# Kernel tuning notes

Hardware: AMD Instinct MI355X
Metric: run time of the kernel (lower is better)

Reference implementation:

```python
import jax, jax.numpy as jnp
import numpy as np

B, L = 4, 1024
D_IN, D_MODEL, DEPTH = 8, 512, 4
D_INNER, D_STATE, D_CONV = 2 * D_MODEL, 16, 4
DT_RANK = (D_MODEL + 15) // 16  # 32


def setup_inputs():
    key = jax.random.key(0)
    ks = jax.random.split(key, 12)
    s = 0.02
    inp = {
        "x": jax.random.normal(ks[0], (B, L, D_IN), jnp.float32),
        "in_w": jax.random.normal(ks[1], (D_MODEL, D_IN), jnp.float32) * s,
        "in_b": jnp.zeros((D_MODEL,), jnp.float32),
        "W_xz": jax.random.normal(ks[2], (DEPTH, 2 * D_INNER, D_MODEL), jnp.float32) * s,
        "conv_w": jax.random.normal(ks[3], (DEPTH, D_INNER, D_CONV), jnp.float32) * 0.1,
        "conv_b": jnp.zeros((DEPTH, D_INNER), jnp.float32),
        "W_xp": jax.random.normal(ks[4], (DEPTH, DT_RANK + 2 * D_STATE, D_INNER), jnp.float32) * s,
        "W_dt": jax.random.normal(ks[5], (DEPTH, D_INNER, DT_RANK), jnp.float32) * 0.1,
        "b_dt": jax.random.uniform(ks[6], (DEPTH, D_INNER), jnp.float32, -4.0, -2.0),
        "A_log": jnp.broadcast_to(jnp.log(jnp.arange(1, D_STATE + 1, dtype=jnp.float32)), (DEPTH, D_INNER, D_STATE)) + 0.0,
        "D_param": jnp.ones((DEPTH, D_INNER), jnp.float32),
        "W_out": jax.random.normal(ks[7], (DEPTH, D_MODEL, D_INNER), jnp.float32) * s,
        "ln_g": jnp.ones((D_MODEL,), jnp.float32),
        "ln_b": jnp.zeros((D_MODEL,), jnp.float32),
    }
    return inp


def _silu(x):
    return x * jax.nn.sigmoid(x)


def _mamba_layer(h, Wxz, cw, cb, Wxp, Wdt, bdt, A_log, Dp, Wout):
    # in_proj -> (x, z)
    xz = jnp.einsum('bld,ed->ble', h, Wxz)           # (B,L,2*D_INNER)
    xc, z = jnp.split(xz, 2, axis=-1)
    # causal depthwise conv1d, kernel D_CONV
    xp = jnp.pad(xc, ((0, 0), (D_CONV - 1, 0), (0, 0)))
    xconv = sum(xp[:, k:k + L, :] * cw[:, k] for k in range(D_CONV)) + cb
    u = _silu(xconv)                                 # (B,L,D_INNER)
    # x_proj -> dt, B, C
    xdbl = jnp.einsum('bld,ed->ble', u, Wxp)
    dt_lr = xdbl[..., :DT_RANK]
    Bm = xdbl[..., DT_RANK:DT_RANK + D_STATE]        # (B,L,D_STATE)
    Cm = xdbl[..., DT_RANK + D_STATE:]               # (B,L,D_STATE)
    dt = jax.nn.softplus(jnp.einsum('blr,dr->bld', dt_lr, Wdt) + bdt)  # (B,L,D_INNER)
    A = -jnp.exp(A_log)                              # (D_INNER,D_STATE)

    def step(hst, inp):
        dt_t, B_t, C_t, u_t = inp                    # (B,Di),(B,S),(B,S),(B,Di)
        dA = jnp.exp(dt_t[..., None] * A)            # (B,Di,S)
        dBu = dt_t[..., None] * B_t[:, None, :] * u_t[..., None]
        hst = dA * hst + dBu
        y_t = jnp.einsum('bds,bs->bd', hst, C_t)
        return hst, y_t

    h0 = jnp.zeros((h.shape[0], D_INNER, D_STATE), h.dtype)
    xs = (dt.transpose(1, 0, 2), Bm.transpose(1, 0, 2), Cm.transpose(1, 0, 2), u.transpose(1, 0, 2))
    _, ys = jax.lax.scan(step, h0, xs)
    y = ys.transpose(1, 0, 2) + u * Dp               # (B,L,D_INNER)
    y = y * _silu(z)
    return jnp.einsum('ble,de->bld', y, Wout)


def reference(x, in_w, in_b, W_xz, conv_w, conv_b, W_xp, W_dt, b_dt, A_log, D_param, W_out, ln_g, ln_b):
    h = jnp.einsum('bli,di->bld', x, in_w) + in_b
    for i in range(DEPTH):
        h = _mamba_layer(h, W_xz[i], conv_w[i], conv_b[i], W_xp[i], W_dt[i], b_dt[i], A_log[i], D_param[i], W_out[i])
    mu = h.mean(-1, keepdims=True)
    var = ((h - mu) ** 2).mean(-1, keepdims=True)
    return (h - mu) * jax.lax.rsqrt(var + 1e-5) * ln_g + ln_b
```

## Files before the change

### kernel.cpp

```cpp
#include <hip/hip_runtime.h>
#include <math.h>

#define B_      4
#define L_      1024
#define D_INNC  8
#define DMODEL  512
#define DEPTH_  4
#define DINNER  1024
#define DSTATE  16
#define DCONV   4
#define DTRANK  32
#define MTOT    (B_*L_)
#define CHUNKS  64
#define CLEN    16
#define XPSPLIT 8

typedef float f32x4 __attribute__((ext_vector_type(4)));
typedef short s16x8 __attribute__((ext_vector_type(8)));
typedef unsigned short u16;
typedef unsigned short u16x4v __attribute__((ext_vector_type(4)));

__device__ __forceinline__ u16 f2bf(float v) {
    unsigned b = __float_as_uint(v);
    return (u16)((b + 0x7FFF + ((b >> 16) & 1)) >> 16);
}
__device__ __forceinline__ float bf2f(u16 h) {
    return __uint_as_float((unsigned)h << 16);
}

__global__ __launch_bounds__(256) void in_proj_kernel(
    const float* __restrict__ x, const float* __restrict__ w,
    const float* __restrict__ bias, u16* __restrict__ hb)
{
    int idx = blockIdx.x * 256 + threadIdx.x;
    int m = idx / DMODEL, d = idx % DMODEL;
    const float* xr = x + m * D_INNC;
    const float* wr = w + d * D_INNC;
    float acc = bias[d];
#pragma unroll
    for (int k = 0; k < D_INNC; ++k) acc += xr[k] * wr[k];
    hb[idx] = f2bf(acc);
}

__global__ __launch_bounds__(256) void wconv_kernel(
    const float* __restrict__ W, u16* __restrict__ Wb)
{
    int i = blockIdx.x * 256 + threadIdx.x;
    const float* src = W + (size_t)i * 8;
    float4 f0 = *(const float4*)src;
    float4 f1 = *(const float4*)(src + 4);
    float f[8] = {f0.x,f0.y,f0.z,f0.w,f1.x,f1.y,f1.z,f1.w};
    s16x8 hv;
#pragma unroll
    for (int e = 0; e < 8; ++e) hv[e] = (short)f2bf(f[e]);
    *(s16x8*)(Wb + (size_t)i * 8) = hv;
}

template<int BM, int BN, int MODE>
__global__ __launch_bounds__(256, 2) void gemm_bf16(
    const u16* __restrict__ A, int lda,
    const u16* __restrict__ B, int ldb,
    void* __restrict__ C0, void* __restrict__ C1,
    int ldc, int K)
{
    constexpr int FM  = BM / 32;
    constexpr int FN  = BN / 32;
    constexpr int ACH = BM / 64;
    constexpr int BCH = BN / 64;
    __shared__ __align__(16) u16 As[4*(BM+1)*8];
    __shared__ __align__(16) u16 Bs[4*(BN+1)*8];

    const int t    = threadIdx.x;
    const int lane = t & 63;
    const int w    = t >> 6;
    const int wm   = (w >> 1) * (BM / 2);
    const int wn   = (w & 1) * (BN / 2);
    const int quad = lane >> 4;
    const int l16  = lane & 15;
    const int m0   = blockIdx.y * BM;
    const int n0   = (MODE == 6) ? 0 : blockIdx.x * BN;
    const int kbase= (MODE == 6) ? blockIdx.x * K : 0;

    f32x4 acc[FM][FN];
#pragma unroll
    for (int i = 0; i < FM; ++i)
#pragma unroll
        for (int j = 0; j < FN; ++j) acc[i][j] = (f32x4){0.f,0.f,0.f,0.f};

    s16x8 ra[ACH], rb[BCH];
#pragma unroll
    for (int c = 0; c < ACH; ++c) {
        int id = c*256 + t, row = id >> 2, kb = id & 3;
        ra[c] = *(const s16x8*)(A + (size_t)(m0 + row) * lda + kbase + kb*8);
    }
#pragma unroll
    for (int c = 0; c < BCH; ++c) {
        int id = c*256 + t, row = id >> 2, kb = id & 3;
        rb[c] = *(const s16x8*)(B + (size_t)(n0 + row) * ldb + kbase + kb*8);
    }

    for (int kk = 0; kk < K; kk += 32) {
        __syncthreads();
#pragma unroll
        for (int c = 0; c < ACH; ++c) {
            int id = c*256 + t, row = id >> 2, kb = id & 3;
            *(s16x8*)&As[(kb*(BM+1) + row) * 8] = ra[c];
        }
#pragma unroll
        for (int c = 0; c < BCH; ++c) {
            int id = c*256 + t, row = id >> 2, kb = id & 3;
            *(s16x8*)&Bs[(kb*(BN+1) + row) * 8] = rb[c];
        }
        __syncthreads();
        int kn = kk + 32;
        if (kn < K) {
#pragma unroll
            for (int c = 0; c < ACH; ++c) {
                int id = c*256 + t, row = id >> 2, kb = id & 3;
                ra[c] = *(const s16x8*)(A + (size_t)(m0 + row) * lda + kbase + kn + kb*8);
            }
#pragma unroll
            for (int c = 0; c < BCH; ++c) {
                int id = c*256 + t, row = id >> 2, kb = id & 3;
                rb[c] = *(const s16x8*)(B + (size_t)(n0 + row) * ldb + kbase + kn + kb*8);
            }
        }
        s16x8 afr[FM], bfr[FN];
#pragma unroll
        for (int i = 0; i < FM; ++i)
            afr[i] = *(const s16x8*)&As[(quad*(BM+1) + wm + i*16 + l16) * 8];
#pragma unroll
        for (int j = 0; j < FN; ++j)
            bfr[j] = *(const s16x8*)&Bs[(quad*(BN+1) + wn + j*16 + l16) * 8];
#pragma unroll
        for (int i = 0; i < FM; ++i)
#pragma unroll
            for (int j = 0; j < FN; ++j)
                acc[i][j] = __builtin_amdgcn_mfma_f32_16x16x32_bf16(afr[i], bfr[j], acc[i][j], 0, 0, 0);
    }

    if constexpr (MODE == 2) {
        u16* C = (u16*)C0;
#pragma unroll
        for (int i = 0; i < FM; ++i)
#pragma unroll
            for (int j = 0; j < FN; ++j) {
                int col = n0 + wn + j*16 + l16;
#pragma unroll
                for (int r = 0; r < 4; ++r) {
                    int row = m0 + wm + i*16 + quad*4 + r;
                    C[(size_t)row * ldc + col] = f2bf(acc[i][j][r]);
                }
            }
    } else if constexpr (MODE == 6) {
        float* P = (float*)C0 + (size_t)blockIdx.x * MTOT * 64;
#pragma unroll
        for (int i = 0; i < FM; ++i)
#pragma unroll
            for (int j = 0; j < FN; ++j) {
                int col = wn + j*16 + l16;
#pragma unroll
                for (int r = 0; r < 4; ++r) {
                    int row = m0 + wm + i*16 + quad*4 + r;
                    P[(size_t)row * 64 + col] = acc[i][j][r];
                }
            }
    } else if constexpr (MODE == 4) {
        u16* dtb_ = (u16*)C0;
        const float* bdt = (const float*)C1;
#pragma unroll
        for (int i = 0; i < FM; ++i)
#pragma unroll
            for (int j = 0; j < FN; ++j) {
                int col = n0 + wn + j*16 + l16;
                float bb = bdt[col];
#pragma unroll
                for (int r = 0; r < 4; ++r) {
                    int row = m0 + wm + i*16 + quad*4 + r;
                    float v = acc[i][j][r] + bb;
                    float sp = (v > 20.f) ? v : log1pf(__expf(v));
                    dtb_[(size_t)row * ldc + col] = f2bf(sp);
                }
            }
    } else {
        u16* xcb = (u16*)C0;
        u16* szb = (u16*)C1;
#pragma unroll
        for (int i = 0; i < FM; ++i)
#pragma unroll
            for (int j = 0; j < FN; ++j) {
                int col = n0 + wn + j*16 + l16;
                bool isz = col >= DINNER;
                int cc = col & (DINNER - 1);
                u16* dst = isz ? szb : xcb;
#pragma unroll
                for (int r = 0; r < 4; ++r) {
                    int row = m0 + wm + i*16 + quad*4 + r;
                    float v = acc[i][j][r];
                    if (isz) v = v / (1.f + __expf(-v));
                    dst[(size_t)row * DINNER + cc] = f2bf(v);
                }
            }
    }
}

__global__ __launch_bounds__(256) void xpred_kernel(
    const float* __restrict__ part, u16* __restrict__ dtlr,
    float* __restrict__ xd)
{
    int tid = blockIdx.x * 256 + threadIdx.x;
    int m = tid >> 4, c4 = (tid & 15) * 4;
    float s0 = 0.f, s1 = 0.f, s2 = 0.f, s3 = 0.f;
#pragma unroll
    for (int p = 0; p < XPSPLIT; ++p) {
        float4 v = *(const float4*)&part[((size_t)p * MTOT + m) * 64 + c4];
        s0 += v.x; s1 += v.y; s2 += v.z; s3 += v.w;
    }
    if (c4 < 32) {
        u16x4v o;
        o[0] = f2bf(s0); o[1] = f2bf(s1); o[2] = f2bf(s2); o[3] = f2bf(s3);
        *(u16x4v*)&dtlr[(size_t)m * 32 + c4] = o;
    } else {
        float4 o; o.x = s0; o.y = s1; o.z = s2; o.w = s3;
        *(float4*)&xd[(size_t)m * 64 + c4] = o;
    }
}

__global__ __launch_bounds__(256) void conv_silu_kernel(
    const u16* __restrict__ xcb, const float* __restrict__ cw,
    const float* __restrict__ cb, u16* __restrict__ ub)
{
    int idx = (blockIdx.x * 256 + threadIdx.x) * 2;
    int m = idx >> 10;
    int d = idx & (DINNER - 1);
    int l = m & (L_ - 1);

    const float4 w0 = *(const float4*)&cw[d * 4];
    const float4 w1 = *(const float4*)&cw[(d + 1) * 4];
    float a0 = cb[d], a1 = cb[d + 1];
#pragma unroll
    for (int k = 0; k < 4; ++k) {
        int lag = 3 - k;
        if (l >= lag) {
            unsigned v = *(const unsigned*)&xcb[(size_t)(m - lag) * DINNER + d];
            float x0 = bf2f((u16)(v & 0xffff));
            float x1 = bf2f((u16)(v >> 16));
            float wk0 = (&w0.x)[k], wk1 = (&w1.x)[k];
            a0 += x0 * wk0; a1 += x1 * wk1;
        }
    }
    a0 = a0 / (1.f + __expf(-a0));
    a1 = a1 / (1.f + __expf(-a1));
    unsigned pack = (unsigned)f2bf(a0) | ((unsigned)f2bf(a1) << 16);
    *(unsigned*)&ub[idx] = pack;
}

__global__ __launch_bounds__(256) void scan1_kernel(
    const u16* __restrict__ ub, const float* xdbl,
    const u16* __restrict__ dtb, const float* __restrict__ A_log,
    u16* __restrict__ hfinal, float* __restrict__ dsum)
{
    __shared__ float Bs[CLEN][16];
    const int blk  = blockIdx.x;
    const int dblk = blk & 3;
    const int c    = (blk >> 2) & (CHUNKS - 1);
    const int b    = blk >> 8;
    const int d    = dblk * 256 + threadIdx.x;
    const int mbase = b * L_ + c * CLEN;

    {
        int idx = threadIdx.x;
        int tt = idx >> 4, ss = idx & 15;
        Bs[tt][ss] = xdbl[(size_t)(mbase + tt) * 64 + 32 + ss];
    }
    float A[16];
    {
        float4 a4[4];
#pragma unroll
        for (int q = 0; q < 4; ++q) a4[q] = *(const float4*)&A_log[d * 16 + q * 4];
        const float* af = (const float*)a4;
#pragma unroll
        for (int s = 0; s < 16; ++s) A[s] = -__expf(af[s]);
    }
    __syncthreads();

    float h[16];
#pragma unroll
    for (int s = 0; s < 16; ++s) h[s] = 0.f;
    float dts = 0.f;

    for (int t0 = 0; t0 < CLEN; t0 += 8) {
        float dt8[8], u8[8];
#pragma unroll
        for (int j = 0; j < 8; ++j) {
            int m = mbase + t0 + j;
            dt8[j] = bf2f(dtb[(size_t)m * DINNER + d]);
            u8[j]  = bf2f(ub [(size_t)m * DINNER + d]);
        }
#pragma unroll
        for (int j = 0; j < 8; ++j) {
            float dtv = dt8[j], dtu = dtv * u8[j];
            dts += dtv;
            float Bt[16];
#pragma unroll
            for (int q = 0; q < 4; ++q)
                *(float4*)&Bt[q*4] = *(const float4*)&Bs[t0 + j][q*4];
#pragma unroll
            for (int s = 0; s < 16; ++s) {
                float dA = __expf(dtv * A[s]);
                h[s] = dA * h[s] + dtu * Bt[s];
            }
        }
    }
    size_t base = ((size_t)(b * CHUNKS + c) * DINNER + d) * 16;
    s16x8 p0, p1;
#pragma unroll
    for (int s = 0; s < 8; ++s) { p0[s] = (short)f2bf(h[s]); p1[s] = (short)f2bf(h[s+8]); }
    *(s16x8*)&hfinal[base]     = p0;
    *(s16x8*)&hfinal[base + 8] = p1;
    dsum[(size_t)(b * CHUNKS + c) * DINNER + d] = dts;
}

__global__ __launch_bounds__(256) void scan2_kernel(
    u16* __restrict__ hfinal, const float* __restrict__ dsum,
    const float* __restrict__ A_log)
{
    int t = blockIdx.x * 256 + threadIdx.x;
    int s = t & 15, d = (t >> 4) & (DINNER - 1), b = t >> 14;
    float As = -__expf(A_log[d * DSTATE + s]);
    float h = 0.f;
    for (int c0 = 0; c0 < CHUNKS; c0 += 8) {
        float hf8[8], dts8[8];
#pragma unroll
        for (int j = 0; j < 8; ++j) {
            int c = c0 + j;
            size_t i = (size_t)(b * CHUNKS + c) * DINNER + d;
            dts8[j] = dsum[i];
            hf8[j]  = bf2f(hfinal[i * 16 + s]);
        }
#pragma unroll
        for (int j = 0; j < 8; ++j) {
            int c = c0 + j;
            size_t idx = ((size_t)(b * CHUNKS + c) * DINNER + d) * 16 + s;
            hfinal[idx] = f2bf(h);
            h = __expf(As * dts8[j]) * h + hf8[j];
        }
    }
}

__global__ __launch_bounds__(256) void scan3_kernel(
    const u16* __restrict__ szb, const u16* __restrict__ ub,
    const float* xdbl, const u16* __restrict__ dtb,
    const float* __restrict__ A_log, const float* __restrict__ Dp,
    const u16* __restrict__ hstart, u16* __restrict__ yb)
{
    __shared__ float Bs[CLEN][16];
    __shared__ float Cs[CLEN][16];
    const int blk  = blockIdx.x;
    const int dblk = blk & 3;
    const int c    = (blk >> 2) & (CHUNKS - 1);
    const int b    = blk >> 8;
    const int d    = dblk * 256 + threadIdx.x;
    const int mbase = b * L_ + c * CLEN;

    {
        int idx = threadIdx.x;
        int tt = idx >> 4, ss = idx & 15;
        Bs[tt][ss] = xdbl[(size_t)(mbase + tt) * 64 + 32 + ss];
        Cs[tt][ss] = xdbl[(size_t)(mbase + tt) * 64 + 48 + ss];
    }
    float A[16];
    {
        float4 a4[4];
#pragma unroll
        for (int q = 0; q < 4; ++q) a4[q] = *(const float4*)&A_log[d * 16 + q * 4];
        const float* af = (const float*)a4;
#pragma unroll
        for (int s = 0; s < 16; ++s) A[s] = -__expf(af[s]);
    }
    const float Dval = Dp[d];

    float h[16];
    {
        size_t base = ((size_t)(b * CHUNKS + c) * DINNER + d) * 16;
        s16x8 p0 = *(const s16x8*)&hstart[base];
        s16x8 p1 = *(const s16x8*)&hstart[base + 8];
#pragma unroll
        for (int s = 0; s < 8; ++s) { h[s] = bf2f((u16)p0[s]); h[s+8] = bf2f((u16)p1[s]); }
    }
    __syncthreads();

    for (int t0 = 0; t0 < CLEN; t0 += 8) {
        float dt8[8], u8[8], sz8[8];
#pragma unroll
        for (int j = 0; j < 8; ++j) {
            int m = mbase + t0 + j;
            dt8[j] = bf2f(dtb[(size_t)m * DINNER + d]);
            u8[j]  = bf2f(ub [(size_t)m * DINNER + d]);
            sz8[j] = bf2f(szb[(size_t)m * DINNER + d]);
        }
#pragma unroll
        for (int j = 0; j < 8; ++j) {
            float dtv = dt8[j], dtu = dtv * u8[j];
            float Bt[16], Ct[16];
#pragma unroll
            for (int q = 0; q < 4; ++q) {
                *(float4*)&Bt[q*4] = *(const float4*)&Bs[t0 + j][q*4];
                *(float4*)&Ct[q*4] = *(const float4*)&Cs[t0 + j][q*4];
            }
            float yv = 0.f;
#pragma unroll
            for (int s = 0; s < 16; ++s) {
                float dA = __expf(dtv * A[s]);
                h[s] = dA * h[s] + dtu * Bt[s];
                yv += h[s] * Ct[s];
            }
            int m = mbase + t0 + j;
            yb[(size_t)m * DINNER + d] = f2bf((yv + u8[j] * Dval) * sz8[j]);
        }
    }
}

__global__ __launch_bounds__(256) void ln_kernel(
    const u16* __restrict__ hb, const float* __restrict__ g,
    const float* __restrict__ bta, float* __restrict__ out)
{
    int m = blockIdx.x;
    size_t base = (size_t)m * DMODEL;
    int t = threadIdx.x;
    float v0 = bf2f(hb[base + t]);
    float v1 = bf2f(hb[base + t + 256]);
    float sum = v0 + v1, sq = v0*v0 + v1*v1;
#pragma unroll
    for (int off = 32; off; off >>= 1) {
        sum += __shfl_down(sum, off);
        sq  += __shfl_down(sq,  off);
    }
    __shared__ float ls[4], lq[4];
    int w = t >> 6;
    if ((t & 63) == 0) { ls[w] = sum; lq[w] = sq; }
    __syncthreads();
    sum = ls[0] + ls[1] + ls[2] + ls[3];
    sq  = lq[0] + lq[1] + lq[2] + lq[3];
    float mu  = sum * (1.f / DMODEL);
    float var = sq * (1.f / DMODEL) - mu * mu;
    float rs  = rsqrtf(var + 1e-5f);
    out[base + t]       = (v0 - mu) * rs * g[t]       + bta[t];
    out[base + t + 256] = (v1 - mu) * rs * g[t + 256] + bta[t + 256];
}

extern "C" void kernel_launch(void* const* d_in, const int* in_sizes, int n_in,
                              void* d_out, int out_size, void* d_ws, size_t ws_size,
                              hipStream_t stream)
{
    const float* x      = (const float*)d_in[0];
    const float* in_w   = (const float*)d_in[1];
    const float* in_b   = (const float*)d_in[2];
    const float* W_xz   = (const float*)d_in[3];
    const float* conv_w = (const float*)d_in[4];
    const float* conv_b = (const float*)d_in[5];
    const float* W_xp   = (const float*)d_in[6];
    const float* W_dt   = (const float*)d_in[7];
    const float* b_dt   = (const float*)d_in[8];
    const float* A_log  = (const float*)d_in[9];
    const float* D_par  = (const float*)d_in[10];
    const float* W_out  = (const float*)d_in[11];
    const float* ln_g   = (const float*)d_in[12];
    const float* ln_b   = (const float*)d_in[13];
    float* out = (float*)d_out;

    float* ws      = (float*)d_ws;
    float* hbF     = ws;
    float* hfinF   = hbF    + 1048576;
    float* xcbF    = hfinF  + 2097152;
    float* szbF    = xcbF   + 2097152;
    float* ubF     = szbF   + 2097152;
    float* xdbl    = ubF    + 2097152;
    float* dtbF    = xdbl   + 262144;
    float* ybF     = dtbF   + 2097152;
    float* wxzF    = ybF    + 2097152;
    float* woutF   = wxzF   + 2097152;
    float* wxpF    = woutF  + 1048576;
    float* wdtF    = wxpF   + 131072;
    float* dsum    = wdtF   + 65536;
    float* dtlrF   = dsum   + 262144;
    float* xpart   = dtlrF  + 65536;

    u16* hb     = (u16*)hbF;
    u16* hfinal = (u16*)hfinF;
    u16* xcb  = (u16*)xcbF;
    u16* szb  = (u16*)szbF;
    u16* ub   = (u16*)ubF;
    u16* dtb  = (u16*)dtbF;
    u16* yb   = (u16*)ybF;
    u16* wxzb  = (u16*)wxzF;
    u16* woutb = (u16*)woutF;
    u16* wxpb  = (u16*)wxpF;
    u16* wdtb  = (u16*)wdtF;
    u16* dtlrb = (u16*)dtlrF;

    wconv_kernel<<<(DEPTH_*2048*DMODEL/8)/256, 256, 0, stream>>>(W_xz, wxzb);
    wconv_kernel<<<(DEPTH_*DMODEL*DINNER/8)/256, 256, 0, stream>>>(W_out, woutb);
    wconv_kernel<<<(DEPTH_*64*DINNER/8)/256, 256, 0, stream>>>(W_xp, wxpb);
    wconv_kernel<<<(DEPTH_*DINNER*DTRANK/8)/256, 256, 0, stream>>>(W_dt, wdtb);

    in_proj_kernel<<<MTOT*DMODEL/256, 256, 0, stream>>>(x, in_w, in_b, hb);

    for (int layer = 0; layer < DEPTH_; ++layer) {
        const float* cw    = conv_w + (size_t)layer * DINNER * DCONV;
        const float* cb    = conv_b + (size_t)layer * DINNER;
        const float* bdt   = b_dt   + (size_t)layer * DINNER;
        const float* Alog  = A_log  + (size_t)layer * DINNER * DSTATE;
        const float* Dp    = D_par  + (size_t)layer * DINNER;
        const u16* wxzL    = wxzb  + (size_t)layer * 2048 * DMODEL;
        const u16* woutL   = woutb + (size_t)layer * DMODEL * DINNER;
        const u16* wxpL    = wxpb  + (size_t)layer * 64 * DINNER;
        const u16* wdtL    = wdtb  + (size_t)layer * DINNER * DTRANK;

        gemm_bf16<128,128,1><<<dim3(2048/128, MTOT/128), 256, 0, stream>>>(
            hb, DMODEL, wxzL, DMODEL, xcb, szb, 0, DMODEL);
        conv_silu_kernel<<<MTOT*DINNER/2/256, 256, 0, stream>>>(xcb, cw, cb, ub);
        gemm_bf16<64,64,6><<<dim3(XPSPLIT, MTOT/64), 256, 0, stream>>>(
            ub, DINNER, wxpL, DINNER, xpart, nullptr, 0, DINNER/XPSPLIT);
        xpred_kernel<<<MTOT*16/256, 256, 0, stream>>>(xpart, dtlrb, xdbl);
        gemm_bf16<64,64,4><<<dim3(DINNER/64, MTOT/64), 256, 0, stream>>>(
            dtlrb, DTRANK, wdtL, DTRANK, dtb, (void*)bdt, DINNER, DTRANK);
        scan1_kernel<<<B_*CHUNKS*(DINNER/256), 256, 0, stream>>>(ub, xdbl, dtb, Alog, hfinal, dsum);
        scan2_kernel<<<(B_*DINNER*DSTATE)/256, 256, 0, stream>>>(hfinal, dsum, Alog);
        scan3_kernel<<<B_*CHUNKS*(DINNER/256), 256, 0, stream>>>(szb, ub, xdbl, dtb, Alog, Dp, hfinal, yb);
        gemm_bf16<64,64,2><<<dim3(DMODEL/64, MTOT/64), 256, 0, stream>>>(
            yb, DINNER, woutL, DINNER, hb, nullptr, DMODEL, DINNER);
    }

    ln_kernel<<<MTOT, 256, 0, stream>>>(hb, ln_g, ln_b, out);
}
```

Before: 593.8 us.

## Stage GEMM tiles via direct global-to-LDS loads with double-buffered swizzled LDS

The bf16 MFMA GEMM now loads A and B tiles straight into LDS with global_load_lds, instead of loading into registers and then storing to LDS. LDS is double-buffered, so the next K-slice is fetched while MFMAs run on the current one, and one barrier per iteration is dropped. An XOR swizzle on the 16-byte k-chunks replaces the old +1 row padding to avoid LDS bank conflicts. The aim is to cut register pressure and LDS store traffic and to overlap loads with compute. The cost is twice the LDS footprint and a dependence on the compiler placing correct vmcnt waits before the barrier.

```diff
diff --git a/kernel.cpp b/kernel.cpp
--- a/kernel.cpp
+++ b/kernel.cpp
@@ -20,6 +20,9 @@
 typedef unsigned short u16;
 typedef unsigned short u16x4v __attribute__((ext_vector_type(4)));
 
+#define GLOBAL_AS __attribute__((address_space(1)))
+#define LDS_AS    __attribute__((address_space(3)))
+
 __device__ __forceinline__ u16 f2bf(float v) {
     unsigned b = __float_as_uint(v);
     return (u16)((b + 0x7FFF + ((b >> 16) & 1)) >> 16);
@@ -56,6 +59,24 @@
     *(s16x8*)(Wb + (size_t)i * 8) = hv;
 }
 
+template<int ROWS>
+__device__ __forceinline__ void stage_tile(
+    const u16* __restrict__ src, int ld, int koff, u16* lds, int t)
+{
+    const int l = t & 63, w = t >> 6;
+    const int r_in = l >> 2, s = l & 3;
+#pragma unroll
+    for (int p = 0; p < ROWS / 64; ++p) {
+        int rb = (p * 4 + w) * 16;
+        int r  = rb + r_in;
+        int sw = s ^ ((r ^ (r >> 2)) & 3);
+        const u16* g = src + (size_t)r * ld + koff + sw * 8;
+        u16* lp = lds + rb * 32;
+        __builtin_amdgcn_global_load_lds(
+            (const GLOBAL_AS void*)g, (LDS_AS void*)lp, 16, 0, 0);
+    }
+}
+
 template<int BM, int BN, int MODE>
 __global__ __launch_bounds__(256, 2) void gemm_bf16(
     const u16* __restrict__ A, int lda,
@@ -63,12 +84,10 @@
     void* __restrict__ C0, void* __restrict__ C1,
     int ldc, int K)
 {
-    constexpr int FM  = BM / 32;
-    constexpr int FN  = BN / 32;
-    constexpr int ACH = BM / 64;
-    constexpr int BCH = BN / 64;
-    __shared__ __align__(16) u16 As[4*(BM+1)*8];
-    __shared__ __align__(16) u16 Bs[4*(BN+1)*8];
+    constexpr int FM = BM / 32;
+    constexpr int FN = BN / 32;
+    __shared__ __align__(16) u16 As[2][BM * 32];
+    __shared__ __align__(16) u16 Bs[2][BN * 32];
 
     const int t    = threadIdx.x;
     const int lane = t & 63;
@@ -80,6 +99,10 @@
     const int m0   = blockIdx.y * BM;
     const int n0   = (MODE == 6) ? 0 : blockIdx.x * BN;
     const int kbase= (MODE == 6) ? blockIdx.x * K : 0;
+    const int sq   = (quad ^ ((l16 ^ (l16 >> 2)) & 3)) * 8;
+
+    const u16* Abase = A + (size_t)m0 * lda;
+    const u16* Bbase = B + (size_t)n0 * ldb;
 
     f32x4 acc[FM][FN];
 #pragma unroll
@@ -87,56 +110,34 @@
 #pragma unroll
         for (int j = 0; j < FN; ++j) acc[i][j] = (f32x4){0.f,0.f,0.f,0.f};
 
-    s16x8 ra[ACH], rb[BCH];
-#pragma unroll
-    for (int c = 0; c < ACH; ++c) {
-        int id = c*256 + t, row = id >> 2, kb = id & 3;
-        ra[c] = *(const s16x8*)(A + (size_t)(m0 + row) * lda + kbase + kb*8);
-    }
-#pragma unroll
-    for (int c = 0; c < BCH; ++c) {
-        int id = c*256 + t, row = id >> 2, kb = id & 3;
-        rb[c] = *(const s16x8*)(B + (size_t)(n0 + row) * ldb + kbase + kb*8);
-    }
-
+    stage_tile<BM>(Abase, lda, kbase, As[0], t);
+    stage_tile<BN>(Bbase, ldb, kbase, Bs[0], t);
+
+    int cur = 0;
     for (int kk = 0; kk < K; kk += 32) {
-        __syncthreads();
-#pragma unroll
-        for (int c = 0; c < ACH; ++c) {
-            int id = c*256 + t, row = id >> 2, kb = id & 3;
-            *(s16x8*)&As[(kb*(BM+1) + row) * 8] = ra[c];
-        }
-#pragma unroll
-        for (int c = 0; c < BCH; ++c) {
-            int id = c*256 + t, row = id >> 2, kb = id & 3;
-            *(s16x8*)&Bs[(kb*(BN+1) + row) * 8] = rb[c];
-        }
         __syncthreads();
         int kn = kk + 32;
         if (kn < K) {
-#pragma unroll
-            for (int c = 0; c < ACH; ++c) {
-                int id = c*256 + t, row = id >> 2, kb = id & 3;
-                ra[c] = *(const s16x8*)(A + (size_t)(m0 + row) * lda + kbase + kn + kb*8);
-            }
-#pragma unroll
-            for (int c = 0; c < BCH; ++c) {
-                int id = c*256 + t, row = id >> 2, kb = id & 3;
-                rb[c] = *(const s16x8*)(B + (size_t)(n0 + row) * ldb + kbase + kn + kb*8);
-            }
+            stage_tile<BM>(Abase, lda, kbase + kn, As[cur ^ 1], t);
+            stage_tile<BN>(Bbase, ldb, kbase + kn, Bs[cur ^ 1], t);
         }
         s16x8 afr[FM], bfr[FN];
 #pragma unroll
-        for (int i = 0; i < FM; ++i)
-            afr[i] = *(const s16x8*)&As[(quad*(BM+1) + wm + i*16 + l16) * 8];
-#pragma unroll
-        for (int j = 0; j < FN; ++j)
-            bfr[j] = *(const s16x8*)&Bs[(quad*(BN+1) + wn + j*16 + l16) * 8];
+        for (int i = 0; i < FM; ++i) {
+            int row = wm + i * 16 + l16;
+            afr[i] = *(const s16x8*)&As[cur][row * 32 + sq];
+        }
+#pragma unroll
+        for (int j = 0; j < FN; ++j) {
+            int row = wn + j * 16 + l16;
+            bfr[j] = *(const s16x8*)&Bs[cur][row * 32 + sq];
+        }
 #pragma unroll
         for (int i = 0; i < FM; ++i)
 #pragma unroll
             for (int j = 0; j < FN; ++j)
                 acc[i][j] = __builtin_amdgcn_mfma_f32_16x16x32_bf16(afr[i], bfr[j], acc[i][j], 0, 0, 0);
+        cur ^= 1;
     }
 
     if constexpr (MODE == 2) {
```

Result: no change. 598.8 us (+0.8%).
